# Performance work log

Hardware: AMD Instinct MI355X
Metric: run time of the kernel (lower is better)

Reference implementation:

```python
import jax, jax.numpy as jnp
import numpy as np

BETA = 0.1
GAMMA = 0.5
LABEL_SMOOTHING = 0.0
IGNORE_INDEX = -100

B, T, H, V = 8, 512, 2048, 32000  # B = 2 * num_pairs (first half chosen, second half rejected)


def setup_inputs() -> dict:
    key = jax.random.key(0)
    k1, k2, k3, k4 = jax.random.split(key, 4)
    lin_weight = jax.random.normal(k1, (V, H), dtype=jnp.float32) * 0.02
    _input = jax.random.normal(k2, (B, T, H), dtype=jnp.float32)
    target = jax.random.randint(k3, (B, T), 0, V, dtype=jnp.int64)
    # sprinkle some ignore_index positions like padded labels
    pad = jax.random.uniform(k4, (B, T)) < 0.1
    target = jnp.where(pad, IGNORE_INDEX, target)
    bias = jax.random.normal(k4, (V,), dtype=jnp.float32) * 0.02
    return {"lin_weight": lin_weight, "_input": _input, "target": target, "bias": bias}


def reference(lin_weight, _input, target, bias):
    # fused linear -> log_softmax over vocab
    logits = jnp.einsum("bth,vh->btv", _input, lin_weight) + bias  # (B, T, V)
    logps = jax.nn.log_softmax(logits.astype(jnp.float32), axis=-1)
    # gather target log-probs, masking ignore_index
    mask = (target != IGNORE_INDEX)
    tgt = jnp.where(mask, target, 0)
    per_token_logps = jnp.take_along_axis(logps, tgt[..., None], axis=-1)[..., 0]
    per_token_logps = per_token_logps * mask  # (B, T)
    # SimPO uses length-normalized (average) sequence log-prob
    avg_logps = per_token_logps.sum(-1) / jnp.maximum(mask.sum(-1), 1)  # (B,)
    n_pairs = B // 2
    chosen_logps = avg_logps[:n_pairs]
    rejected_logps = avg_logps[n_pairs:]
    d = BETA * (chosen_logps - rejected_logps) - GAMMA
    loss = (-jax.nn.log_sigmoid(d) * (1.0 - LABEL_SMOOTHING)
            - jax.nn.log_sigmoid(-d) * LABEL_SMOOTHING).sum() / n_pairs
    return loss
```

## Files before the change

kernel.cpp:

```cpp
#include <hip/hip_runtime.h>
#include <stdint.h>
#include <math.h>

constexpr int Bb = 8, Tt = 512, Hh = 2048, Vv = 32000;
constexpr int M = Bb * Tt;
constexpr int K = Hh;
constexpr int N = Vv;
constexpr int BM = 256, BN = 256, BK = 64;
constexpr int MBLK = M / BM;
constexpr int NBLK = N / BN;
constexpr int KTILES = K / BK;
constexpr int IGNORE = -100;

typedef __attribute__((ext_vector_type(8))) short bf16x8;
typedef __attribute__((ext_vector_type(4))) float f32x4;

__device__ inline void gld16(const void* g, void* l) {
  __builtin_amdgcn_global_load_lds(
      (const __attribute__((address_space(1))) uint32_t*)g,
      (__attribute__((address_space(3))) uint32_t*)l, 16, 0, 0);
}

__device__ __forceinline__ void barrier_f() {
  asm volatile("" ::: "memory");
  __builtin_amdgcn_s_barrier();
  asm volatile("" ::: "memory");
}

__device__ inline unsigned short f2bf(float f) {
  union { float f; unsigned u; } x; x.f = f;
  unsigned r = x.u + 0x7fffu + ((x.u >> 16) & 1u);
  return (unsigned short)(r >> 16);
}

__global__ void cast_bf16_kernel(const float* __restrict__ src,
                                 unsigned short* __restrict__ dst, int n4) {
  int i = blockIdx.x * blockDim.x + threadIdx.x;
  int stride = gridDim.x * blockDim.x;
  const float4* s4 = (const float4*)src;
  ushort4* d4 = (ushort4*)dst;
  for (; i < n4; i += stride) {
    float4 v = s4[i];
    ushort4 o;
    o.x = f2bf(v.x); o.y = f2bf(v.y); o.z = f2bf(v.z); o.w = f2bf(v.w);
    d4[i] = o;
  }
}


template <int BUF, int KS, int MH, int VM, class STG>
__device__ __forceinline__ void phase(const unsigned short* __restrict__ AsB,
                                      const unsigned short* __restrict__ BsB,
                                      const int* offA, const int* offB,
                                      bf16x8 (&bfrag)[4], f32x4 (&acc)[8][4],
                                      STG&& stg) {
  const unsigned short* Ab = AsB + (BUF * 2 + KS) * 8192;
  if (MH == 0) {
    const unsigned short* Bp = BsB + (BUF * 2 + KS) * 8192;
#pragma unroll
    for (int nf = 0; nf < 4; ++nf) bfrag[nf] = *(const bf16x8*)(Bp + offB[nf]);
  }
  bf16x8 af[4];
#pragma unroll
  for (int mi = 0; mi < 4; ++mi) af[mi] = *(const bf16x8*)(Ab + offA[MH * 4 + mi]);
  stg();
  if (VM == 4) asm volatile("s_waitcnt vmcnt(4)" ::: "memory");
  if (VM == 0) asm volatile("s_waitcnt vmcnt(0)" ::: "memory");
  barrier_f();
  asm volatile("s_waitcnt lgkmcnt(0)" ::: "memory");
  __builtin_amdgcn_s_setprio(1);
#pragma unroll
  for (int mi = 0; mi < 4; ++mi)
#pragma unroll
    for (int nf = 0; nf < 4; ++nf)
      acc[MH * 4 + mi][nf] = __builtin_amdgcn_mfma_f32_16x16x32_bf16(
          af[mi], bfrag[nf], acc[MH * 4 + mi][nf], 0, 0, 0);
  __builtin_amdgcn_s_setprio(0);
  barrier_f();
}

__global__ __launch_bounds__(512, 2)
void gemm_stats(const unsigned short* __restrict__ X,
                const unsigned short* __restrict__ W,
                const float* __restrict__ bias,
                const int* __restrict__ tgt,
                float* __restrict__ m_part,
                float* __restrict__ s_part,
                float* __restrict__ tlogit) {
  extern __shared__ unsigned short smem[];
  unsigned short* AsB = smem;
  unsigned short* BsB = smem + 32768;
  float* red_m = (float*)(smem + 65536);
  float* red_s = red_m + 1024;

  const int tid = threadIdx.x;
  const int lane = tid & 63;
  const int wid = tid >> 6;
  const int waveM = wid >> 2;
  const int waveN = wid & 3;
  const int q = lane >> 4;
  const int c = lane & 15;

  const int swz = (blockIdx.x & 7) * (MBLK * NBLK / 8) + (blockIdx.x >> 3);
  const int bm = swz & (MBLK - 1);
  const int bn = swz >> 4;

  const int srow = tid >> 2;
  const int sch = (lane & 3) ^ ((lane >> 3) & 3);
  const unsigned short* gA = X + (size_t)(bm * BM + srow) * K + sch * 8;
  const unsigned short* gB = W + (size_t)(bn * BN + srow) * K + sch * 8;
  unsigned short* const dA0 = AsB + wid * 512;
  unsigned short* const dB0 = BsB + wid * 512;

  auto stA = [&](int b, int h, int t) {
    const unsigned short* s = gA + t * BK + h * 32;
    unsigned short* d = dA0 + (b * 2 + h) * 8192;
    gld16(s, d);
    gld16(s + (size_t)128 * K, d + 4096);
  };
  auto stB = [&](int b, int h, int t) {
    const unsigned short* s = gB + t * BK + h * 32;
    unsigned short* d = dB0 + (b * 2 + h) * 8192;
    gld16(s, d);
    gld16(s + (size_t)128 * K, d + 4096);
  };

  const int chrd = (q ^ ((c >> 1) & 3)) * 8;
  int offA[8], offB[4];
#pragma unroll
  for (int mf = 0; mf < 8; ++mf) offA[mf] = (waveM * 128 + mf * 16 + c) * 32 + chrd;
#pragma unroll
  for (int nf = 0; nf < 4; ++nf) offB[nf] = (waveN * 64 + nf * 16 + c) * 32 + chrd;

  f32x4 acc[8][4];
#pragma unroll
  for (int i = 0; i < 8; ++i)
#pragma unroll
    for (int j = 0; j < 4; ++j) acc[i][j] = (f32x4){0.f, 0.f, 0.f, 0.f};
  bf16x8 bfrag[4];

  stA(0, 0, 0); stB(0, 0, 0);
  stA(0, 1, 0); stB(0, 1, 0);
  stA(1, 0, 1); stB(1, 0, 1);
  asm volatile("s_waitcnt vmcnt(4)" ::: "memory");
  barrier_f();

  for (int i = 0; i < KTILES / 2 - 1; ++i) {
    const int t0 = 2 * i;
    phase<0, 0, 0, -1>(AsB, BsB, offA, offB, bfrag, acc, [&] { stA(1, 1, t0 + 1); });
    phase<0, 0, 1, -1>(AsB, BsB, offA, offB, bfrag, acc, [&] { stB(1, 1, t0 + 1); });
    phase<0, 1, 0, -1>(AsB, BsB, offA, offB, bfrag, acc, [&] { stA(0, 0, t0 + 2); });
    phase<0, 1, 1,  4>(AsB, BsB, offA, offB, bfrag, acc, [&] { stB(0, 0, t0 + 2); });
    phase<1, 0, 0, -1>(AsB, BsB, offA, offB, bfrag, acc, [&] { stA(0, 1, t0 + 2); });
    phase<1, 0, 1, -1>(AsB, BsB, offA, offB, bfrag, acc, [&] { stB(0, 1, t0 + 2); });
    phase<1, 1, 0, -1>(AsB, BsB, offA, offB, bfrag, acc, [&] { stA(1, 0, t0 + 3); });
    phase<1, 1, 1,  4>(AsB, BsB, offA, offB, bfrag, acc, [&] { stB(1, 0, t0 + 3); });
  }
  {
    auto nop = [&] {};
    phase<0, 0, 0, -1>(AsB, BsB, offA, offB, bfrag, acc, [&] { stA(1, 1, KTILES - 1); });
    phase<0, 0, 1, -1>(AsB, BsB, offA, offB, bfrag, acc, [&] { stB(1, 1, KTILES - 1); });
    phase<0, 1, 0, -1>(AsB, BsB, offA, offB, bfrag, acc, nop);
    phase<0, 1, 1,  0>(AsB, BsB, offA, offB, bfrag, acc, nop);
    phase<1, 0, 0, -1>(AsB, BsB, offA, offB, bfrag, acc, nop);
    phase<1, 0, 1, -1>(AsB, BsB, offA, offB, bfrag, acc, nop);
    phase<1, 1, 0, -1>(AsB, BsB, offA, offB, bfrag, acc, nop);
    phase<1, 1, 1, -1>(AsB, BsB, offA, offB, bfrag, acc, nop);
  }

  const int colBase = bn * BN + waveN * 64;
  float bvals[4];
#pragma unroll
  for (int nf = 0; nf < 4; ++nf) bvals[nf] = bias[colBase + nf * 16 + c];

#pragma unroll
  for (int mf = 0; mf < 8; ++mf) {
    const int rowBase = bm * BM + waveM * 128 + mf * 16 + q * 4;
#pragma unroll
    for (int reg = 0; reg < 4; ++reg) {
      const int grow = rowBase + reg;
      const int t = tgt[grow];
      float v[4];
      float mloc = -3.4e38f;
#pragma unroll
      for (int nf = 0; nf < 4; ++nf) {
        v[nf] = acc[mf][nf][reg] + bvals[nf];
        mloc = fmaxf(mloc, v[nf]);
        if (colBase + nf * 16 + c == t) tlogit[grow] = v[nf];
      }
#pragma unroll
      for (int off = 1; off < 16; off <<= 1) mloc = fmaxf(mloc, __shfl_xor(mloc, off));
      float sloc = 0.f;
#pragma unroll
      for (int nf = 0; nf < 4; ++nf) sloc += __expf(v[nf] - mloc);
#pragma unroll
      for (int off = 1; off < 16; off <<= 1) sloc += __shfl_xor(sloc, off);
      if (c == 0) {
        const int lrow = waveM * 128 + mf * 16 + q * 4 + reg;
        red_m[waveN * 256 + lrow] = mloc;
        red_s[waveN * 256 + lrow] = sloc;
      }
    }
  }
  __syncthreads();
  if (tid < 256) {
    const float m0 = red_m[tid],       m1 = red_m[256 + tid];
    const float m2 = red_m[512 + tid], m3 = red_m[768 + tid];
    const float mx = fmaxf(fmaxf(m0, m1), fmaxf(m2, m3));
    const float ss = red_s[tid] * __expf(m0 - mx) + red_s[256 + tid] * __expf(m1 - mx) +
                     red_s[512 + tid] * __expf(m2 - mx) + red_s[768 + tid] * __expf(m3 - mx);
    const int grow = bm * BM + tid;
    m_part[(size_t)grow * NBLK + bn] = mx;
    s_part[(size_t)grow * NBLK + bn] = ss;
  }
}

__global__ __launch_bounds__(256)
void combine_rows(const float* __restrict__ m_part, const float* __restrict__ s_part,
                  const float* __restrict__ tlogit, const int* __restrict__ tgt,
                  float* __restrict__ logp) {
  const int row = blockIdx.x * 4 + (threadIdx.x >> 6);
  const int lane = threadIdx.x & 63;
  const float* mrow = m_part + (size_t)row * NBLK;
  const float* srow = s_part + (size_t)row * NBLK;
  const bool v1 = (lane + 64) < NBLK;
  const float m0 = mrow[lane];
  const float s0 = srow[lane];
  const float m1 = v1 ? mrow[lane + 64] : -3.4e38f;
  const float s1 = v1 ? srow[lane + 64] : 0.f;
  float mx = fmaxf(m0, m1);
#pragma unroll
  for (int off = 32; off >= 1; off >>= 1) mx = fmaxf(mx, __shfl_xor(mx, off));
  float s = s0 * __expf(m0 - mx) + s1 * __expf(m1 - mx);
#pragma unroll
  for (int off = 32; off >= 1; off >>= 1) s += __shfl_xor(s, off);
  if (lane == 0) {
    const int t = tgt[row];
    logp[row] = (t == IGNORE) ? 0.f : (tlogit[row] - mx - logf(s));
  }
}

__global__ void finalize(const float* __restrict__ logp, const int* __restrict__ tgt,
                         float* __restrict__ out) {
  __shared__ float avg[8];
  const int w = threadIdx.x >> 6;
  const int lane = threadIdx.x & 63;
  float s = 0.f, cnt = 0.f;
  for (int i = lane; i < Tt; i += 64) {
    const int idx = w * Tt + i;
    s += logp[idx];
    cnt += (tgt[idx] != IGNORE) ? 1.f : 0.f;
  }
#pragma unroll
  for (int off = 32; off >= 1; off >>= 1) {
    s += __shfl_xor(s, off);
    cnt += __shfl_xor(cnt, off);
  }
  if (lane == 0) avg[w] = s / fmaxf(cnt, 1.f);
  __syncthreads();
  if (threadIdx.x == 0) {
    float loss = 0.f;
#pragma unroll
    for (int p = 0; p < 4; ++p) {
      const float d = 0.1f * (avg[p] - avg[p + 4]) - 0.5f;
      const float nl = (d > 0.f) ? log1pf(expf(-d)) : (-d + log1pf(expf(d)));
      loss += nl;
    }
    out[0] = loss * 0.25f;
  }
}

extern "C" void kernel_launch(void* const* d_in, const int* in_sizes, int n_in,
                              void* d_out, int out_size, void* d_ws, size_t ws_size,
                              hipStream_t stream) {
  const float* Wf   = (const float*)d_in[0];
  const float* Xf   = (const float*)d_in[1];
  const int*   tgt  = (const int*)d_in[2];
  const float* bias = (const float*)d_in[3];
  float* out = (float*)d_out;

  char* ws = (char*)d_ws;
  size_t off = 0;
  auto alloc = [&](size_t bytes) {
    void* p = ws + off;
    off += (bytes + 255) & ~(size_t)255;
    return p;
  };
  unsigned short* Xbf = (unsigned short*)alloc((size_t)M * K * 2);
  unsigned short* Wbf = (unsigned short*)alloc((size_t)N * K * 2);
  float* m_part = (float*)alloc((size_t)M * NBLK * 4);
  float* s_part = (float*)alloc((size_t)M * NBLK * 4);
  float* tlog   = (float*)alloc((size_t)M * 4);
  float* logp   = (float*)alloc((size_t)M * 4);

  cast_bf16_kernel<<<2048, 256, 0, stream>>>(Xf, Xbf, M * K / 4);
  cast_bf16_kernel<<<8192, 256, 0, stream>>>(Wf, Wbf, N * K / 4);

  constexpr size_t SMEM = 2u * 2u * 256u * 32u * 2u * 2u
                        + 2u * 4u * 256u * 4u;
  gemm_stats<<<dim3(MBLK * NBLK), dim3(512), SMEM, stream>>>(
      Xbf, Wbf, bias, tgt, m_part, s_part, tlog);

  combine_rows<<<M / 4, 256, 0, stream>>>(m_part, s_part, tlog, tgt, logp);
  finalize<<<1, 512, 0, stream>>>(logp, tgt, out);
}
```

Before: 908.0 us.

## Make GEMM-stats kernel persistent and prefetch next tile during epilogue

The fused GEMM plus softmax-statistics kernel now launches 256 persistent blocks instead of one block per output tile. Each block walks its XCD's tile range with a stride of 32 tiles. During the last K-phases of each tile it issues global-to-LDS loads for the first K-tiles of the next tile, so those loads overlap the row max and sum epilogue. This removes per-block launch and prologue latency, at the cost of more complex control flow and some imbalance, since blocks process either 7 or 8 tiles.

```diff
diff --git a/kernel.cpp b/kernel.cpp
--- a/kernel.cpp
+++ b/kernel.cpp
@@ -10,6 +10,8 @@
 constexpr int MBLK = M / BM;
 constexpr int NBLK = N / BN;
 constexpr int KTILES = K / BK;
+constexpr int TILES = MBLK * NBLK;
+constexpr int TPX = TILES / 8;
 constexpr int IGNORE = -100;
 
 typedef __attribute__((ext_vector_type(8))) short bf16x8;
@@ -101,36 +103,46 @@
   const int q = lane >> 4;
   const int c = lane & 15;
 
-  const int swz = (blockIdx.x & 7) * (MBLK * NBLK / 8) + (blockIdx.x >> 3);
-  const int bm = swz & (MBLK - 1);
-  const int bn = swz >> 4;
+  const int xcd = blockIdx.x & 7;
+  const int local = blockIdx.x >> 3;
 
   const int srow = tid >> 2;
   const int sch = (lane & 3) ^ ((lane >> 3) & 3);
+  unsigned short* const dA0 = AsB + wid * 512;
+  unsigned short* const dB0 = BsB + wid * 512;
+
+  auto stAp = [&](const unsigned short* g, int bf, int h, int kt) {
+    const unsigned short* sp = g + kt * BK + h * 32;
+    unsigned short* d = dA0 + (bf * 2 + h) * 8192;
+    gld16(sp, d);
+    gld16(sp + (size_t)128 * K, d + 4096);
+  };
+  auto stBp = [&](const unsigned short* g, int bf, int h, int kt) {
+    const unsigned short* sp = g + kt * BK + h * 32;
+    unsigned short* d = dB0 + (bf * 2 + h) * 8192;
+    gld16(sp, d);
+    gld16(sp + (size_t)128 * K, d + 4096);
+  };
+
+  const int chrd = (q ^ ((c >> 1) & 3)) * 8;
+  int offA[8], offB[4];
+#pragma unroll
+  for (int mf = 0; mf < 8; ++mf) offA[mf] = (waveM * 128 + mf * 16 + c) * 32 + chrd;
+#pragma unroll
+  for (int nf = 0; nf < 4; ++nf) offB[nf] = (waveN * 64 + nf * 16 + c) * 32 + chrd;
+
+  int s = local;
+  int swz = xcd * TPX + s;
+  int bm = swz & (MBLK - 1);
+  int bn = swz >> 4;
   const unsigned short* gA = X + (size_t)(bm * BM + srow) * K + sch * 8;
   const unsigned short* gB = W + (size_t)(bn * BN + srow) * K + sch * 8;
-  unsigned short* const dA0 = AsB + wid * 512;
-  unsigned short* const dB0 = BsB + wid * 512;
-
-  auto stA = [&](int b, int h, int t) {
-    const unsigned short* s = gA + t * BK + h * 32;
-    unsigned short* d = dA0 + (b * 2 + h) * 8192;
-    gld16(s, d);
-    gld16(s + (size_t)128 * K, d + 4096);
-  };
-  auto stB = [&](int b, int h, int t) {
-    const unsigned short* s = gB + t * BK + h * 32;
-    unsigned short* d = dB0 + (b * 2 + h) * 8192;
-    gld16(s, d);
-    gld16(s + (size_t)128 * K, d + 4096);
-  };
-
-  const int chrd = (q ^ ((c >> 1) & 3)) * 8;
-  int offA[8], offB[4];
-#pragma unroll
-  for (int mf = 0; mf < 8; ++mf) offA[mf] = (waveM * 128 + mf * 16 + c) * 32 + chrd;
-#pragma unroll
-  for (int nf = 0; nf < 4; ++nf) offB[nf] = (waveN * 64 + nf * 16 + c) * 32 + chrd;
+
+  stAp(gA, 0, 0, 0); stBp(gB, 0, 0, 0);
+  stAp(gA, 0, 1, 0); stBp(gB, 0, 1, 0);
+  stAp(gA, 1, 0, 1); stBp(gB, 1, 0, 1);
+  asm volatile("s_waitcnt vmcnt(4)" ::: "memory");
+  barrier_f();
 
   f32x4 acc[8][4];
 #pragma unroll
@@ -139,79 +151,110 @@
     for (int j = 0; j < 4; ++j) acc[i][j] = (f32x4){0.f, 0.f, 0.f, 0.f};
   bf16x8 bfrag[4];
 
-  stA(0, 0, 0); stB(0, 0, 0);
-  stA(0, 1, 0); stB(0, 1, 0);
-  stA(1, 0, 1); stB(1, 0, 1);
-  asm volatile("s_waitcnt vmcnt(4)" ::: "memory");
-  barrier_f();
-
-  for (int i = 0; i < KTILES / 2 - 1; ++i) {
-    const int t0 = 2 * i;
-    phase<0, 0, 0, -1>(AsB, BsB, offA, offB, bfrag, acc, [&] { stA(1, 1, t0 + 1); });
-    phase<0, 0, 1, -1>(AsB, BsB, offA, offB, bfrag, acc, [&] { stB(1, 1, t0 + 1); });
-    phase<0, 1, 0, -1>(AsB, BsB, offA, offB, bfrag, acc, [&] { stA(0, 0, t0 + 2); });
-    phase<0, 1, 1,  4>(AsB, BsB, offA, offB, bfrag, acc, [&] { stB(0, 0, t0 + 2); });
-    phase<1, 0, 0, -1>(AsB, BsB, offA, offB, bfrag, acc, [&] { stA(0, 1, t0 + 2); });
-    phase<1, 0, 1, -1>(AsB, BsB, offA, offB, bfrag, acc, [&] { stB(0, 1, t0 + 2); });
-    phase<1, 1, 0, -1>(AsB, BsB, offA, offB, bfrag, acc, [&] { stA(1, 0, t0 + 3); });
-    phase<1, 1, 1,  4>(AsB, BsB, offA, offB, bfrag, acc, [&] { stB(1, 0, t0 + 3); });
-  }
-  {
-    auto nop = [&] {};
-    phase<0, 0, 0, -1>(AsB, BsB, offA, offB, bfrag, acc, [&] { stA(1, 1, KTILES - 1); });
-    phase<0, 0, 1, -1>(AsB, BsB, offA, offB, bfrag, acc, [&] { stB(1, 1, KTILES - 1); });
-    phase<0, 1, 0, -1>(AsB, BsB, offA, offB, bfrag, acc, nop);
-    phase<0, 1, 1,  0>(AsB, BsB, offA, offB, bfrag, acc, nop);
-    phase<1, 0, 0, -1>(AsB, BsB, offA, offB, bfrag, acc, nop);
-    phase<1, 0, 1, -1>(AsB, BsB, offA, offB, bfrag, acc, nop);
-    phase<1, 1, 0, -1>(AsB, BsB, offA, offB, bfrag, acc, nop);
-    phase<1, 1, 1, -1>(AsB, BsB, offA, offB, bfrag, acc, nop);
-  }
-
-  const int colBase = bn * BN + waveN * 64;
-  float bvals[4];
-#pragma unroll
-  for (int nf = 0; nf < 4; ++nf) bvals[nf] = bias[colBase + nf * 16 + c];
-
-#pragma unroll
-  for (int mf = 0; mf < 8; ++mf) {
-    const int rowBase = bm * BM + waveM * 128 + mf * 16 + q * 4;
-#pragma unroll
-    for (int reg = 0; reg < 4; ++reg) {
-      const int grow = rowBase + reg;
-      const int t = tgt[grow];
-      float v[4];
-      float mloc = -3.4e38f;
-#pragma unroll
-      for (int nf = 0; nf < 4; ++nf) {
-        v[nf] = acc[mf][nf][reg] + bvals[nf];
-        mloc = fmaxf(mloc, v[nf]);
-        if (colBase + nf * 16 + c == t) tlogit[grow] = v[nf];
+  while (true) {
+    const bool last = (s + 32 >= TPX);
+
+    for (int i = 0; i < KTILES / 2 - 1; ++i) {
+      const int t0 = 2 * i;
+      phase<0, 0, 0, -1>(AsB, BsB, offA, offB, bfrag, acc, [&] { stAp(gA, 1, 1, t0 + 1); });
+      phase<0, 0, 1, -1>(AsB, BsB, offA, offB, bfrag, acc, [&] { stBp(gB, 1, 1, t0 + 1); });
+      phase<0, 1, 0, -1>(AsB, BsB, offA, offB, bfrag, acc, [&] { stAp(gA, 0, 0, t0 + 2); });
+      phase<0, 1, 1,  4>(AsB, BsB, offA, offB, bfrag, acc, [&] { stBp(gB, 0, 0, t0 + 2); });
+      phase<1, 0, 0, -1>(AsB, BsB, offA, offB, bfrag, acc, [&] { stAp(gA, 0, 1, t0 + 2); });
+      phase<1, 0, 1, -1>(AsB, BsB, offA, offB, bfrag, acc, [&] { stBp(gB, 0, 1, t0 + 2); });
+      phase<1, 1, 0, -1>(AsB, BsB, offA, offB, bfrag, acc, [&] { stAp(gA, 1, 0, t0 + 3); });
+      phase<1, 1, 1,  4>(AsB, BsB, offA, offB, bfrag, acc, [&] { stBp(gB, 1, 0, t0 + 3); });
+    }
+
+    const unsigned short* gA_n = gA;
+    const unsigned short* gB_n = gB;
+    if (!last) {
+      const int swz_n = swz + 32;
+      const int bm_n = swz_n & (MBLK - 1);
+      const int bn_n = swz_n >> 4;
+      gA_n = X + (size_t)(bm_n * BM + srow) * K + sch * 8;
+      gB_n = W + (size_t)(bn_n * BN + srow) * K + sch * 8;
+      phase<0, 0, 0, -1>(AsB, BsB, offA, offB, bfrag, acc, [&] { stAp(gA, 1, 1, KTILES - 1); });
+      phase<0, 0, 1, -1>(AsB, BsB, offA, offB, bfrag, acc, [&] { stBp(gB, 1, 1, KTILES - 1); });
+      phase<0, 1, 0, -1>(AsB, BsB, offA, offB, bfrag, acc, [&] { stAp(gA_n, 0, 0, 0); });
+      phase<0, 1, 1,  4>(AsB, BsB, offA, offB, bfrag, acc, [&] { stBp(gB_n, 0, 0, 0); });
+      phase<1, 0, 0, -1>(AsB, BsB, offA, offB, bfrag, acc, [&] { stAp(gA_n, 0, 1, 0); });
+      phase<1, 0, 1, -1>(AsB, BsB, offA, offB, bfrag, acc, [&] { stBp(gB_n, 0, 1, 0); });
+      phase<1, 1, 0, -1>(AsB, BsB, offA, offB, bfrag, acc, [&] { stAp(gA_n, 1, 0, 1); });
+      phase<1, 1, 1,  4>(AsB, BsB, offA, offB, bfrag, acc, [&] { stBp(gB_n, 1, 0, 1); });
+    } else {
+      auto nop = [&] {};
+      phase<0, 0, 0, -1>(AsB, BsB, offA, offB, bfrag, acc, [&] { stAp(gA, 1, 1, KTILES - 1); });
+      phase<0, 0, 1, -1>(AsB, BsB, offA, offB, bfrag, acc, [&] { stBp(gB, 1, 1, KTILES - 1); });
+      phase<0, 1, 0, -1>(AsB, BsB, offA, offB, bfrag, acc, nop);
+      phase<0, 1, 1,  0>(AsB, BsB, offA, offB, bfrag, acc, nop);
+      phase<1, 0, 0, -1>(AsB, BsB, offA, offB, bfrag, acc, nop);
+      phase<1, 0, 1, -1>(AsB, BsB, offA, offB, bfrag, acc, nop);
+      phase<1, 1, 0, -1>(AsB, BsB, offA, offB, bfrag, acc, nop);
+      phase<1, 1, 1, -1>(AsB, BsB, offA, offB, bfrag, acc, nop);
+    }
+
+    {
+      const int colBase = bn * BN + waveN * 64;
+      float bvals[4];
+#pragma unroll
+      for (int nf = 0; nf < 4; ++nf) bvals[nf] = bias[colBase + nf * 16 + c];
+
+#pragma unroll
+      for (int mf = 0; mf < 8; ++mf) {
+        const int rowBase = bm * BM + waveM * 128 + mf * 16 + q * 4;
+#pragma unroll
+        for (int reg = 0; reg < 4; ++reg) {
+          const int grow = rowBase + reg;
+          const int t = tgt[grow];
+          float v[4];
+          float mloc = -3.4e38f;
+#pragma unroll
+          for (int nf = 0; nf < 4; ++nf) {
+            v[nf] = acc[mf][nf][reg] + bvals[nf];
+            mloc = fmaxf(mloc, v[nf]);
+            if (colBase + nf * 16 + c == t) tlogit[grow] = v[nf];
+          }
+#pragma unroll
+          for (int off = 1; off < 16; off <<= 1) mloc = fmaxf(mloc, __shfl_xor(mloc, off));
+          float sloc = 0.f;
+#pragma unroll
+          for (int nf = 0; nf < 4; ++nf) sloc += __expf(v[nf] - mloc);
+#pragma unroll
+          for (int off = 1; off < 16; off <<= 1) sloc += __shfl_xor(sloc, off);
+          if (c == 0) {
+            const int lrow = waveM * 128 + mf * 16 + q * 4 + reg;
+            red_m[waveN * 256 + lrow] = mloc;
+            red_s[waveN * 256 + lrow] = sloc;
+          }
+        }
       }
-#pragma unroll
-      for (int off = 1; off < 16; off <<= 1) mloc = fmaxf(mloc, __shfl_xor(mloc, off));
-      float sloc = 0.f;
-#pragma unroll
-      for (int nf = 0; nf < 4; ++nf) sloc += __expf(v[nf] - mloc);
-#pragma unroll
-      for (int off = 1; off < 16; off <<= 1) sloc += __shfl_xor(sloc, off);
-      if (c == 0) {
-        const int lrow = waveM * 128 + mf * 16 + q * 4 + reg;
-        red_m[waveN * 256 + lrow] = mloc;
-        red_s[waveN * 256 + lrow] = sloc;
+      asm volatile("s_waitcnt lgkmcnt(0)" ::: "memory");
+      barrier_f();
+      if (tid < 256) {
+        const float m0 = red_m[tid],       m1 = red_m[256 + tid];
+        const float m2 = red_m[512 + tid], m3 = red_m[768 + tid];
+        const float mx = fmaxf(fmaxf(m0, m1), fmaxf(m2, m3));
+        const float ss = red_s[tid] * __expf(m0 - mx) + red_s[256 + tid] * __expf(m1 - mx) +
+                         red_s[512 + tid] * __expf(m2 - mx) + red_s[768 + tid] * __expf(m3 - mx);
+        const int grow = bm * BM + tid;
+        m_part[(size_t)grow * NBLK + bn] = mx;
+        s_part[(size_t)grow * NBLK + bn] = ss;
       }
     }
-  }
-  __syncthreads();
-  if (tid < 256) {
-    const float m0 = red_m[tid],       m1 = red_m[256 + tid];
-    const float m2 = red_m[512 + tid], m3 = red_m[768 + tid];
-    const float mx = fmaxf(fmaxf(m0, m1), fmaxf(m2, m3));
-    const float ss = red_s[tid] * __expf(m0 - mx) + red_s[256 + tid] * __expf(m1 - mx) +
-                     red_s[512 + tid] * __expf(m2 - mx) + red_s[768 + tid] * __expf(m3 - mx);
-    const int grow = bm * BM + tid;
-    m_part[(size_t)grow * NBLK + bn] = mx;
-    s_part[(size_t)grow * NBLK + bn] = ss;
+
+    if (last) break;
+
+    s += 32;
+    swz += 32;
+    bm = swz & (MBLK - 1);
+    bn = swz >> 4;
+    gA = gA_n;
+    gB = gB_n;
+#pragma unroll
+    for (int i = 0; i < 8; ++i)
+#pragma unroll
+      for (int j = 0; j < 4; ++j) acc[i][j] = (f32x4){0.f, 0.f, 0.f, 0.f};
   }
 }
 
@@ -298,7 +341,7 @@
 
   constexpr size_t SMEM = 2u * 2u * 256u * 32u * 2u * 2u
                         + 2u * 4u * 256u * 4u;
-  gemm_stats<<<dim3(MBLK * NBLK), dim3(512), SMEM, stream>>>(
+  gemm_stats<<<dim3(256), dim3(512), SMEM, stream>>>(
       Xbf, Wbf, bias, tgt, m_part, s_part, tlog);
 
   combine_rows<<<M / 4, 256, 0, stream>>>(m_part, s_part, tlog, tgt, logp);
```

New measurement: 987.1 us. 8.7% more time.
